# Performance work log

Hardware: AMD Instinct MI355X
Metric: run time of the kernel (lower is better)

The kernel has to match this reference:

```python
import jax, jax.numpy as jnp
import numpy as np

BN_EPS = 1e-5
SQ_EPS = 1e-7
NUM_SAMPLES = 4
NUM_CHILD = 8
DIM_CHILD = 8
NUM_PARENT = 8
DIM_PARENT = 16
ROUTING_ITERS = 3
OFFSET_SCALE = 1.0


def squash(x, axis=-1):
    sq = jnp.sum(x * x, axis=axis, keepdims=True)
    return (sq / (1.0 + sq)) * x / jnp.sqrt(sq + SQ_EPS)


def bilinear_sample(feat, grid):
    # feat: [B,C,H,W], grid: [B,H,W,2] in [-1,1], align_corners=True, zeros padding
    B, C, H, W = feat.shape
    x = (grid[..., 0] + 1.0) * 0.5 * (W - 1)
    y = (grid[..., 1] + 1.0) * 0.5 * (H - 1)
    x0 = jnp.floor(x); y0 = jnp.floor(y)
    x1 = x0 + 1.0; y1 = y0 + 1.0
    wx1 = x - x0; wx0 = 1.0 - wx1
    wy1 = y - y0; wy0 = 1.0 - wy1
    featf = feat.reshape(B, C, H * W)

    def gather(xi, yi):
        valid = (xi >= 0) & (xi <= W - 1) & (yi >= 0) & (yi <= H - 1)
        xc = jnp.clip(xi, 0, W - 1).astype(jnp.int32)
        yc = jnp.clip(yi, 0, H - 1).astype(jnp.int32)
        idx = (yc * W + xc).reshape(B, 1, H * W)
        v = jnp.take_along_axis(featf, idx, axis=2).reshape(B, C, H, W)
        return v * valid[:, None].astype(feat.dtype)

    out = (gather(x0, y0) * (wx0 * wy0)[:, None]
           + gather(x1, y0) * (wx1 * wy0)[:, None]
           + gather(x0, y1) * (wx0 * wy1)[:, None]
           + gather(x1, y1) * (wx1 * wy1)[:, None])
    return out


def setup_inputs() -> dict:
    key = jax.random.key(0)
    ks = jax.random.split(key, 8)
    B, C, H, W = 8, 256, 32, 32
    caps_ch = NUM_CHILD * DIM_CHILD  # 64
    return {
        "x": jax.random.normal(ks[0], (B, C, H, W), jnp.float32),
        "primary_w": jax.random.normal(ks[1], (caps_ch, C), jnp.float32) * 0.05,
        "bn_gamma": jnp.ones((caps_ch,), jnp.float32),
        "bn_beta": jnp.zeros((caps_ch,), jnp.float32),
        "bn_mean": jax.random.normal(ks[2], (caps_ch,), jnp.float32) * 0.1,
        "bn_var": jax.random.uniform(ks[3], (caps_ch,), jnp.float32, 0.5, 1.5),
        "offset_w": jax.random.normal(ks[4], (2 * NUM_SAMPLES, C, 3, 3), jnp.float32) * 0.01,
        "offset_b": jnp.zeros((2 * NUM_SAMPLES,), jnp.float32),
        "routing_W": jax.random.normal(ks[5], (NUM_SAMPLES * NUM_CHILD, NUM_PARENT, DIM_PARENT, DIM_CHILD), jnp.float32) * 0.01,
    }


def reference(x, primary_w, bn_gamma, bn_beta, bn_mean, bn_var, offset_w, offset_b, routing_W):
    B, C, H, W = x.shape
    # --- PrimaryCaps: 1x1 conv + BN(inference) + SiLU + squash over capsule dim ---
    p = jnp.einsum('bchw,oc->bohw', x, primary_w)
    p = (p - bn_mean[None, :, None, None]) / jnp.sqrt(bn_var + BN_EPS)[None, :, None, None]
    p = p * bn_gamma[None, :, None, None] + bn_beta[None, :, None, None]
    p = jax.nn.silu(p)
    child = p.reshape(B, NUM_CHILD, DIM_CHILD, H, W)
    child = squash(child, axis=2)
    child_flat = child.reshape(B, NUM_CHILD * DIM_CHILD, H, W)

    # --- Offset conv 3x3, SAME padding ---
    off = jax.lax.conv_general_dilated(x, offset_w, (1, 1), 'SAME',
                                       dimension_numbers=('NCHW', 'OIHW', 'NCHW'))
    off = off + offset_b[None, :, None, None]
    off = off.reshape(B, NUM_SAMPLES, 2, H, W)
    off = jnp.tanh(off) * OFFSET_SCALE
    scale = jnp.array([max(W - 1, 1) / 2.0, max(H - 1, 1) / 2.0], x.dtype).reshape(1, 1, 2, 1, 1)
    off = off / scale

    ys = jnp.linspace(-1.0, 1.0, H, dtype=x.dtype)
    xs = jnp.linspace(-1.0, 1.0, W, dtype=x.dtype)
    yy, xx = jnp.meshgrid(ys, xs, indexing='ij')
    base = jnp.stack((xx, yy), axis=-1)  # [H,W,2]
    grids = base[None, None] + jnp.transpose(off, (0, 1, 3, 4, 2))  # [B,S,H,W,2]

    sampled = jax.vmap(lambda g: bilinear_sample(child_flat, g),
                       in_axes=1, out_axes=1)(grids)  # [B,S,caps_ch,H,W]
    sampled = sampled.reshape(B, NUM_SAMPLES, NUM_CHILD, DIM_CHILD, H, W)
    sampled = jnp.transpose(sampled, (0, 4, 5, 1, 2, 3))  # [B,H,W,S,NC,DC]
    sampled = sampled.reshape(B * H * W, NUM_SAMPLES * NUM_CHILD, DIM_CHILD)

    # --- Dynamic routing ---
    # u_hat: [M, N_in, N_out, D_out]
    u_hat = jnp.einsum('nodi,mni->mnod', routing_W, sampled)
    M = u_hat.shape[0]
    b = jnp.zeros((M, NUM_SAMPLES * NUM_CHILD, NUM_PARENT), x.dtype)
    v = None
    for it in range(ROUTING_ITERS):
        c = jax.nn.softmax(b, axis=-1)
        s = jnp.einsum('mno,mnod->mod', c, u_hat)
        v = squash(s, axis=-1)
        if it < ROUTING_ITERS - 1:
            b = b + jnp.einsum('mnod,mod->mno', u_hat, v)

    routed = v.reshape(B, H, W, NUM_PARENT, DIM_PARENT)
    out = jnp.transpose(routed, (0, 3, 4, 1, 2)).reshape(B, NUM_PARENT * DIM_PARENT, H, W)
    return out
```

## Files before the change

kernel.cpp:

```cpp
#include <hip/hip_runtime.h>
#include <math.h>

#define HW 1024
#define Hd 32
#define Wd 32
#define Bn 8
#define Cc 256

typedef _Float16 half2_t __attribute__((ext_vector_type(2)));
union F2H { float f; half2_t h; };

static __device__ __forceinline__ float dot2(half2_t a, half2_t b, float c) {
#if __has_builtin(__builtin_amdgcn_fdot2)
    return __builtin_amdgcn_fdot2(a, b, c, false);
#else
    return c + (float)a.x * (float)b.x + (float)a.y * (float)b.y;
#endif
}

template<int CTRL>
static __device__ __forceinline__ float dppx(float v) {
    union { float f; int i; } a, r;
    a.f = v;
    r.i = __builtin_amdgcn_update_dpp(0, a.i, CTRL, 0xF, 0xF, true);
    return r.f;
}

__global__ __launch_bounds__(256) void kTPA(const float* __restrict__ x,
        const float* __restrict__ ow, const float* __restrict__ rw,
        const float* __restrict__ pw, const float* __restrict__ gamma,
        const float* __restrict__ beta, const float* __restrict__ mean,
        const float* __restrict__ var,
        float* __restrict__ xt, float* __restrict__ wt2,
        _Float16* __restrict__ wth, float* __restrict__ child_t) {
    __shared__ float lds[20480];
    int bid = blockIdx.x;
    int tid = threadIdx.x;
    if (bid < 512) {
        float (*tile)[65] = (float(*)[65])lds;
        int b = bid >> 6, ct = (bid >> 4) & 3, ht = bid & 15;
        int c0 = ct * 64, hw0 = ht * 64;
        int tr = tid >> 6, tc = tid & 63;
        const float* xb = x + ((size_t)b * 256 + c0) * 1024 + hw0;
        #pragma unroll
        for (int k = 0; k < 16; ++k) {
            int c = tr + k * 4;
            tile[c][tc] = xb[(size_t)c * 1024 + tc];
        }
        __syncthreads();
        float* xo = xt + ((size_t)b * 1024 + hw0) * 256 + c0;
        #pragma unroll
        for (int k = 0; k < 16; ++k) {
            int hwl = tr + k * 4;
            xo[(size_t)hwl * 256 + tc] = tile[tc][hwl];
        }
    } else if (bid < 584) {
        int t = (bid - 512) * 256 + tid;
        int c = t & 255, oc = (t >> 8) & 7, tap = t >> 11;
        wt2[t] = ow[(oc * 256 + c) * 9 + tap];
    } else if (bid < 712) {
        int t = (bid - 584) * 256 + tid;
        int i = t & 7, l = (t >> 3) & 63, j = t >> 9;
        int n = (l & 3) | ((l >> 1) & 0x1C);
        int half = (l >> 2) & 1;
        int o = j >> 4, d = j & 15;
        wth[t] = (_Float16)rw[n * 1024 + half * 512 + o * 128 + d * 8 + i];
    } else {
        float* xs = lds;
        float* wl = lds + 4096;
        {
            const float4* pw4 = reinterpret_cast<const float4*>(pw);
            #pragma unroll
            for (int k = 0; k < 16; ++k) {
                int f = k * 256 + tid;
                float4 v = pw4[f];
                int o = f >> 6, c4 = f & 63;
                *reinterpret_cast<float4*>(
                    wl + c4 * 256 + (((o ^ c4) & 63) << 2)) = v;
            }
        }
        int m0b = (bid - 712) * 16;
        int b = m0b >> 10, hw0 = m0b & 1023;
        {
            int c = tid;
            const float4* xr = reinterpret_cast<const float4*>(
                x + ((size_t)b * 256 + c) * 1024 + hw0);
            float4 q0 = xr[0], q1 = xr[1], q2 = xr[2], q3 = xr[3];
            xs[0 * 256 + c] = q0.x;  xs[1 * 256 + c] = q0.y;
            xs[2 * 256 + c] = q0.z;  xs[3 * 256 + c] = q0.w;
            xs[4 * 256 + c] = q1.x;  xs[5 * 256 + c] = q1.y;
            xs[6 * 256 + c] = q1.z;  xs[7 * 256 + c] = q1.w;
            xs[8 * 256 + c] = q2.x;  xs[9 * 256 + c] = q2.y;
            xs[10 * 256 + c] = q2.z; xs[11 * 256 + c] = q2.w;
            xs[12 * 256 + c] = q3.x; xs[13 * 256 + c] = q3.y;
            xs[14 * 256 + c] = q3.z; xs[15 * 256 + c] = q3.w;
        }
        __syncthreads();
        int wid = tid >> 6, lane = tid & 63;
        int o = lane;
        float scale = gamma[o] * rsqrtf(var[o] + 1e-5f);
        float mn = mean[o], bt = beta[o];
        const float4* wl4 = reinterpret_cast<const float4*>(wl);
        #pragma unroll
        for (int pp = 0; pp < 4; pp += 2) {
            int lp = wid * 4 + pp;
            const float4* xa = reinterpret_cast<const float4*>(xs + lp * 256);
            const float4* xb = reinterpret_cast<const float4*>(xs + (lp + 1) * 256);
            float a0 = 0.f, a1 = 0.f;
            #pragma unroll 8
            for (int c4 = 0; c4 < 64; ++c4) {
                float4 wv = wl4[c4 * 64 + (lane ^ (c4 & 63))];
                float4 v0 = xa[c4], v1 = xb[c4];
                a0 += wv.x * v0.x + wv.y * v0.y + wv.z * v0.z + wv.w * v0.w;
                a1 += wv.x * v1.x + wv.y * v1.y + wv.z * v1.z + wv.w * v1.w;
            }
            #pragma unroll
            for (int e = 0; e < 2; ++e) {
                float acc = e ? a1 : a0;
                float t = (acc - mn) * scale + bt;
                float s = t / (1.f + expf(-t));
                float sq = s * s;
                sq += __shfl_xor(sq, 1);
                sq += __shfl_xor(sq, 2);
                sq += __shfl_xor(sq, 4);
                float f = (sq / (1.f + sq)) * rsqrtf(sq + 1e-7f);
                child_t[(size_t)(m0b + lp + e) * 64 + o] = s * f;
            }
        }
    }
}

__global__ __launch_bounds__(256) void kB(const float* __restrict__ xt,
        const float* __restrict__ wt2, const float* __restrict__ ob,
        float* __restrict__ grids) {
    __shared__ float wl[16384];
    int wid = threadIdx.x >> 6, lane = threadIdx.x & 63;
    {
        const float4* wt24 = reinterpret_cast<const float4*>(wt2);
        float4* wl4w = reinterpret_cast<float4*>(wl);
        #pragma unroll
        for (int k = 0; k < 16; ++k)
            wl4w[k * 256 + threadIdx.x] = wt24[k * 256 + threadIdx.x];
    }
    __syncthreads();

    int m0 = (blockIdx.x * 4 + wid) * 4;
    int b = m0 >> 10, hw0 = m0 & 1023;
    int yy = hw0 >> 5, xx0 = hw0 & 31;
    const float* xb = xt + (size_t)b * HW * 256;

    float acc[4][8];
    #pragma unroll
    for (int px = 0; px < 4; ++px)
        #pragma unroll
        for (int oc = 0; oc < 8; ++oc) acc[px][oc] = 0.f;

    #pragma unroll
    for (int tap = 0; tap < 9; ++tap) {
        int ky = tap / 3 - 1, kx = tap % 3 - 1;
        int yq = yy + ky;
        bool vy = (yq >= 0) && (yq <= Hd - 1);
        float4 xv[4];
        #pragma unroll
        for (int px = 0; px < 4; ++px) {
            int xq = xx0 + px + kx;
            bool ok = vy && (xq >= 0) && (xq <= Wd - 1);
            float4 z; z.x = z.y = z.z = z.w = 0.f;
            xv[px] = ok ? *reinterpret_cast<const float4*>(
                              xb + (size_t)(yq * Wd + xq) * 256 + lane * 4)
                        : z;
        }
        #pragma unroll
        for (int oc = 0; oc < 8; ++oc) {
            float4 wv = (tap < 8)
                ? *reinterpret_cast<const float4*>(wl + (tap * 8 + oc) * 256 + lane * 4)
                : *reinterpret_cast<const float4*>(wt2 + (8 * 8 + oc) * 256 + lane * 4);
            #pragma unroll
            for (int px = 0; px < 4; ++px)
                acc[px][oc] += xv[px].x * wv.x + xv[px].y * wv.y +
                               xv[px].z * wv.z + xv[px].w * wv.w;
        }
    }

    int l0 = lane & 1, l1 = (lane >> 1) & 1;
    int o2 = (lane >> 2) & 1, o3 = (lane >> 3) & 1, o4 = (lane >> 4) & 1;
    float y1[2][8];
    #pragma unroll
    for (int ph = 0; ph < 2; ++ph)
        #pragma unroll
        for (int oc = 0; oc < 8; ++oc) {
            float keep = l0 ? acc[(ph << 1) | 1][oc] : acc[(ph << 1) | 0][oc];
            float send = l0 ? acc[(ph << 1) | 0][oc] : acc[(ph << 1) | 1][oc];
            y1[ph][oc] = keep + dppx<0xB1>(send);
        }
    float y2[8];
    #pragma unroll
    for (int oc = 0; oc < 8; ++oc) {
        float keep = l1 ? y1[1][oc] : y1[0][oc];
        float send = l1 ? y1[0][oc] : y1[1][oc];
        y2[oc] = keep + dppx<0x4E>(send);
    }
    float z4[4];
    #pragma unroll
    for (int oh = 0; oh < 4; ++oh) {
        float keep = o2 ? y2[(oh << 1) | 1] : y2[(oh << 1) | 0];
        float send = o2 ? y2[(oh << 1) | 0] : y2[(oh << 1) | 1];
        z4[oh] = keep + __shfl_xor(send, 4);
    }
    float w2[2];
    #pragma unroll
    for (int oh = 0; oh < 2; ++oh) {
        float keep = o3 ? z4[(oh << 1) | 1] : z4[(oh << 1) | 0];
        float send = o3 ? z4[(oh << 1) | 0] : z4[(oh << 1) | 1];
        w2[oh] = keep + dppx<0x128>(send);
    }
    {
        float keep = o4 ? w2[1] : w2[0];
        float send = o4 ? w2[0] : w2[1];
        float s = keep + __shfl_xor(send, 16);
        s += __shfl_xor(s, 32);
        if (lane < 32) {
            int px = lane & 3, oc = (lane >> 2) & 7;
            float t = tanhf(s + ob[oc]);
            int coord = oc & 1, si = oc >> 1;
            int xx = xx0 + px;
            float base = coord ? (-1.f + yy * (2.f / 31.f))
                               : (-1.f + xx * (2.f / 31.f));
            grids[(size_t)(m0 + px) * 8 + si * 2 + coord] =
                base + t * (1.f / 15.5f);
        }
    }
}

__global__ __launch_bounds__(256, 2) void kD(const float* __restrict__ child_t,
        const float* __restrict__ grids, const _Float16* __restrict__ wth,
        float* __restrict__ out) {
    __shared__ float vband_s[4][128];
    int wid = threadIdx.x >> 6, lane = threadIdx.x & 63;
    float* vband = vband_s[wid];
    int m = blockIdx.x * 4 + wid;
    int b = m >> 10, hw = m & 1023;
    int n = (lane & 3) | ((lane >> 1) & 0x1C);
    int half = (lane >> 2) & 1;
    int si = n >> 3, ch = n & 7;
    int dsl = (n & 1) * 8 + ((n >> 1) & 1) * 4 + ((n >> 2) & 1) * 2 + ((n >> 3) & 1);

    float gx = grids[m * 8 + si * 2 + 0];
    float gy = grids[m * 8 + si * 2 + 1];
    float xf = (gx + 1.f) * 0.5f * 31.f;
    float yf = (gy + 1.f) * 0.5f * 31.f;
    float x0 = floorf(xf), y0 = floorf(yf);
    float wx1 = xf - x0, wx0 = 1.f - wx1;
    float wy1 = yf - y0, wy0 = 1.f - wy1;
    float sf[8] = {0.f, 0.f, 0.f, 0.f, 0.f, 0.f, 0.f, 0.f};
    const float* cb = child_t + (size_t)b * HW * 64 + ch * 8;
    #pragma unroll
    for (int cy = 0; cy < 2; ++cy) {
        float yq = y0 + (float)cy;
        bool vy = (yq >= 0.f) && (yq <= 31.f);
        float wy = cy ? wy1 : wy0;
        #pragma unroll
        for (int cx = 0; cx < 2; ++cx) {
            float xq = x0 + (float)cx;
            bool ok = vy && (xq >= 0.f) && (xq <= 31.f);
            if (!ok) continue;
            float w = wy * (cx ? wx1 : wx0);
            const float* cp = cb + (size_t)((int)yq * Wd + (int)xq) * 64;
            float4 v0 = *reinterpret_cast<const float4*>(cp);
            float4 v1 = *reinterpret_cast<const float4*>(cp + 4);
            sf[0] += w * v0.x; sf[1] += w * v0.y;
            sf[2] += w * v0.z; sf[3] += w * v0.w;
            sf[4] += w * v1.x; sf[5] += w * v1.y;
            sf[6] += w * v1.z; sf[7] += w * v1.w;
        }
    }
    half2_t sh0 = {(_Float16)sf[0], (_Float16)sf[1]};
    half2_t sh1 = {(_Float16)sf[2], (_Float16)sf[3]};
    half2_t sh2 = {(_Float16)sf[4], (_Float16)sf[5]};
    half2_t sh3 = {(_Float16)sf[6], (_Float16)sf[7]};

    __builtin_amdgcn_s_setprio(1);
    float u[4][16];
    const float4* wt4 = reinterpret_cast<const float4*>(wth);
    #pragma unroll
    for (int o = 0; o < 4; ++o) {
        #pragma unroll
        for (int d = 0; d < 16; ++d) {
            float4 wv = wt4[(o * 16 + d) * 64 + lane];
            F2H a0, a1, a2, a3;
            a0.f = wv.x; a1.f = wv.y; a2.f = wv.z; a3.f = wv.w;
            float acc = dot2(a0.h, sh0, 0.f);
            acc = dot2(a1.h, sh1, acc);
            acc = dot2(a2.h, sh2, acc);
            acc = dot2(a3.h, sh3, acc);
            u[o][d] = acc;
        }
    }
    __builtin_amdgcn_s_setprio(0);

    float bl[4] = {0.f, 0.f, 0.f, 0.f};
    #pragma unroll
    for (int it = 0; it < 3; ++it) {
        float ex[4], rs;
        if (it == 0) {
            ex[0] = ex[1] = ex[2] = ex[3] = 1.f;
            rs = 0.125f;
        } else {
            float mx = fmaxf(fmaxf(bl[0], bl[1]), fmaxf(bl[2], bl[3]));
            mx = fmaxf(mx, __shfl_xor(mx, 4));
            float ssum = 0.f;
            #pragma unroll
            for (int k = 0; k < 4; ++k) { ex[k] = expf(bl[k] - mx); ssum += ex[k]; }
            ssum += __shfl_xor(ssum, 4);
            rs = 1.f / ssum;
        }

        float sval[4];
        #pragma unroll
        for (int o = 0; o < 4; ++o) {
            float cc = ex[o] * rs;
            float y[8];
            #pragma unroll
            for (int d = 0; d < 8; ++d) {
                float t = (n & 1) ? cc * u[o][d] : cc * u[o][d + 8];
                float k = (n & 1) ? cc * u[o][d + 8] : cc * u[o][d];
                y[d] = k + dppx<0xB1>(t);
            }
            float z[4];
            #pragma unroll
            for (int d = 0; d < 4; ++d) {
                float t = (n & 2) ? y[d] : y[d + 4];
                float k = (n & 2) ? y[d + 4] : y[d];
                z[d] = k + dppx<0x4E>(t);
            }
            float w2[2];
            #pragma unroll
            for (int d = 0; d < 2; ++d) {
                float t = (n & 4) ? z[d] : z[d + 2];
                float k = (n & 4) ? z[d + 2] : z[d];
                w2[d] = k + dppx<0x128>(t);
            }
            float t4 = (n & 8) ? w2[0] : w2[1];
            float k4 = (n & 8) ? w2[1] : w2[0];
            float s1 = k4 + __shfl_xor(t4, 16);
            s1 += __shfl_xor(s1, 32);
            sval[o] = s1;
        }
        #pragma unroll
        for (int o = 0; o < 4; ++o) {
            float q = sval[o] * sval[o];
            q += dppx<0xB1>(q);
            q += dppx<0x4E>(q);
            q += dppx<0x128>(q);
            q += __shfl_xor(q, 16);
            float f = (q / (1.f + q)) / sqrtf(q + 1e-7f);
            if ((lane & 32) == 0)
                vband[(half * 4 + o) * 16 + dsl] = sval[o] * f;
        }
        if (it < 2) {
            #pragma unroll
            for (int o = 0; o < 4; ++o) {
                const float4* vr = reinterpret_cast<const float4*>(
                    vband + (half * 4 + o) * 16);
                float4 v0 = vr[0], v1 = vr[1], v2 = vr[2], v3 = vr[3];
                float agg = u[o][0] * v0.x + u[o][1] * v0.y +
                            u[o][2] * v0.z + u[o][3] * v0.w +
                            u[o][4] * v1.x + u[o][5] * v1.y +
                            u[o][6] * v1.z + u[o][7] * v1.w +
                            u[o][8] * v2.x + u[o][9] * v2.y +
                            u[o][10] * v2.z + u[o][11] * v2.w +
                            u[o][12] * v3.x + u[o][13] * v3.y +
                            u[o][14] * v3.z + u[o][15] * v3.w;
                bl[o] += agg;
            }
        } else {
            int o_own = lane >> 4;
            int och = half * 4 + o_own;
            int d0 = ((lane & 3) | ((lane >> 1) & 4)) * 2;
            float va = vband[och * 16 + d0 + 0];
            float vb = vband[och * 16 + d0 + 1];
            float* op = out + ((size_t)b * 128 + och * 16) * HW + hw;
            op[(size_t)(d0 + 0) * HW] = va;
            op[(size_t)(d0 + 1) * HW] = vb;
        }
    }
}

extern "C" void kernel_launch(void* const* d_in, const int* in_sizes, int n_in,
                              void* d_out, int out_size, void* d_ws, size_t ws_size,
                              hipStream_t stream) {
    const float* x     = (const float*)d_in[0];
    const float* pw    = (const float*)d_in[1];
    const float* gamma = (const float*)d_in[2];
    const float* beta  = (const float*)d_in[3];
    const float* mean  = (const float*)d_in[4];
    const float* var   = (const float*)d_in[5];
    const float* ow    = (const float*)d_in[6];
    const float* ob    = (const float*)d_in[7];
    const float* rw    = (const float*)d_in[8];
    float* out = (float*)d_out;
    char* ws = (char*)d_ws;
    float*     child_t = (float*)ws;
    float*     grids   = (float*)(ws + 2097152);
    _Float16*  wth     = (_Float16*)(ws + 2359296);
    float*     wt2     = (float*)(ws + 2424832);
    float*     xt      = (float*)(ws + 2498560);

    hipLaunchKernelGGL(kTPA, dim3(1224), dim3(256), 0, stream,
                       x, ow, rw, pw, gamma, beta, mean, var,
                       xt, wt2, wth, child_t);
    hipLaunchKernelGGL(kB, dim3(512), dim3(256), 0, stream,
                       xt, wt2, ob, grids);
    hipLaunchKernelGGL(kD, dim3(2048), dim3(256), 0, stream,
                       child_t, grids, wth, out);
}
```

Baseline: 76.31 us.

## Store routing predictions as packed fp16 pairs and raise kD occupancy to 4 blocks

Holds the 64 per-lane u_hat values as 32 packed half2 registers instead of 64 floats, converting back to float for each use in the routing loop. Launch bounds for kD go from 2 to 4 blocks per CU so the register savings can become more resident waves. This trades extra fp16/fp32 conversions and lower precision of u_hat (adding rounding error to routing) for higher occupancy and better latency hiding of the gather loads.

```diff
diff --git a/kernel.cpp b/kernel.cpp
--- a/kernel.cpp
+++ b/kernel.cpp
@@ -232,7 +232,7 @@
     }
 }
 
-__global__ __launch_bounds__(256, 2) void kD(const float* __restrict__ child_t,
+__global__ __launch_bounds__(256, 4) void kD(const float* __restrict__ child_t,
         const float* __restrict__ grids, const _Float16* __restrict__ wth,
         float* __restrict__ out) {
     __shared__ float vband_s[4][128];
@@ -280,20 +280,27 @@
     half2_t sh3 = {(_Float16)sf[6], (_Float16)sf[7]};
 
     __builtin_amdgcn_s_setprio(1);
-    float u[4][16];
+    half2_t uh[4][8];
     const float4* wt4 = reinterpret_cast<const float4*>(wth);
     #pragma unroll
     for (int o = 0; o < 4; ++o) {
         #pragma unroll
-        for (int d = 0; d < 16; ++d) {
-            float4 wv = wt4[(o * 16 + d) * 64 + lane];
+        for (int d = 0; d < 8; ++d) {
+            float4 wa = wt4[(o * 16 + d) * 64 + lane];
             F2H a0, a1, a2, a3;
-            a0.f = wv.x; a1.f = wv.y; a2.f = wv.z; a3.f = wv.w;
-            float acc = dot2(a0.h, sh0, 0.f);
-            acc = dot2(a1.h, sh1, acc);
-            acc = dot2(a2.h, sh2, acc);
-            acc = dot2(a3.h, sh3, acc);
-            u[o][d] = acc;
+            a0.f = wa.x; a1.f = wa.y; a2.f = wa.z; a3.f = wa.w;
+            float lo = dot2(a0.h, sh0, 0.f);
+            lo = dot2(a1.h, sh1, lo);
+            lo = dot2(a2.h, sh2, lo);
+            lo = dot2(a3.h, sh3, lo);
+            float4 wb = wt4[(o * 16 + d + 8) * 64 + lane];
+            F2H b0, b1, b2, b3;
+            b0.f = wb.x; b1.f = wb.y; b2.f = wb.z; b3.f = wb.w;
+            float hi = dot2(b0.h, sh0, 0.f);
+            hi = dot2(b1.h, sh1, hi);
+            hi = dot2(b2.h, sh2, hi);
+            hi = dot2(b3.h, sh3, hi);
+            uh[o][d] = half2_t{(_Float16)lo, (_Float16)hi};
         }
     }
     __builtin_amdgcn_s_setprio(0);
@@ -322,8 +329,10 @@
             float y[8];
             #pragma unroll
             for (int d = 0; d < 8; ++d) {
-                float t = (n & 1) ? cc * u[o][d] : cc * u[o][d + 8];
-                float k = (n & 1) ? cc * u[o][d + 8] : cc * u[o][d];
+                float lo = (float)uh[o][d].x;
+                float hi = (float)uh[o][d].y;
+                float t = (n & 1) ? cc * lo : cc * hi;
+                float k = (n & 1) ? cc * hi : cc * lo;
                 y[d] = k + dppx<0xB1>(t);
             }
             float z[4];
@@ -363,14 +372,15 @@
                 const float4* vr = reinterpret_cast<const float4*>(
                     vband + (half * 4 + o) * 16);
                 float4 v0 = vr[0], v1 = vr[1], v2 = vr[2], v3 = vr[3];
-                float agg = u[o][0] * v0.x + u[o][1] * v0.y +
-                            u[o][2] * v0.z + u[o][3] * v0.w +
-                            u[o][4] * v1.x + u[o][5] * v1.y +
-                            u[o][6] * v1.z + u[o][7] * v1.w +
-                            u[o][8] * v2.x + u[o][9] * v2.y +
-                            u[o][10] * v2.z + u[o][11] * v2.w +
-                            u[o][12] * v3.x + u[o][13] * v3.y +
-                            u[o][14] * v3.z + u[o][15] * v3.w;
+                float vv[16] = {v0.x, v0.y, v0.z, v0.w, v1.x, v1.y, v1.z, v1.w,
+                                v2.x, v2.y, v2.z, v2.w, v3.x, v3.y, v3.z, v3.w};
+                float agg = 0.f;
+                #pragma unroll
+                for (int d = 0; d < 8; ++d) {
+                    float lo = (float)uh[o][d].x;
+                    float hi = (float)uh[o][d].y;
+                    agg += lo * vv[d] + hi * vv[d + 8];
+                }
                 bl[o] += agg;
             }
         } else {
```

New measurement: 174.1 us. 128% more time.
